# Optimization experiments

Measured on AMD Instinct MI355X. Metric: run time of the kernel, lower is better.

Reference implementation:

```python
import jax, jax.numpy as jnp
import numpy as np

B, S, D_IN, D_EMB, H = 2, 2048, 1024, 1024, 16
HD = D_EMB // H  # projection_dim = 64


def setup_inputs() -> dict:
    key = jax.random.key(0)
    ks = jax.random.split(key, 9)
    s_in = 1.0 / np.sqrt(D_IN)
    s_emb = 1.0 / np.sqrt(D_EMB)
    return {
        "inputs": jax.random.normal(ks[0], (B, S, D_IN), dtype=jnp.float32),
        "Wq": jax.random.uniform(ks[1], (D_IN, D_EMB), jnp.float32, -s_in, s_in),
        "bq": jax.random.uniform(ks[2], (D_EMB,), jnp.float32, -s_in, s_in),
        "Wk": jax.random.uniform(ks[3], (D_IN, D_EMB), jnp.float32, -s_in, s_in),
        "bk": jax.random.uniform(ks[4], (D_EMB,), jnp.float32, -s_in, s_in),
        "Wv": jax.random.uniform(ks[5], (D_IN, D_EMB), jnp.float32, -s_in, s_in),
        "bv": jax.random.uniform(ks[6], (D_EMB,), jnp.float32, -s_in, s_in),
        "Wo": jax.random.uniform(ks[7], (D_EMB, D_EMB), jnp.float32, -s_emb, s_emb),
        "bo": jax.random.uniform(ks[8], (D_EMB,), jnp.float32, -s_emb, s_emb),
    }


def reference(inputs, Wq, bq, Wk, bk, Wv, bv, Wo, bo):
    b, s, _ = inputs.shape
    # QKV projections -> [b, h, s, hd]
    def split_heads(x):
        return x.reshape(b, s, H, HD).transpose(0, 2, 1, 3)
    q = split_heads(inputs @ Wq + bq)
    k = split_heads(inputs @ Wk + bk)
    v = split_heads(inputs @ Wv + bv)
    scale = 1.0 / jnp.sqrt(jnp.float32(HD))
    logits = jnp.einsum('bhqd,bhkd->bhqk', q, k) * scale
    attn = jax.nn.softmax(logits, axis=-1)
    ctx = jnp.einsum('bhqk,bhkd->bhqd', attn, v)  # [b,h,s,hd]
    concat = ctx.transpose(0, 2, 1, 3).reshape(b, s, D_EMB)
    return concat @ Wo + bo
```

## Files before the change

### kernel.cpp

```cpp
#include <hip/hip_runtime.h>
#include <stdint.h>

#define S_ 2048
#define H_ 16

typedef short s16x8 __attribute__((ext_vector_type(8)));
typedef float f32x4 __attribute__((ext_vector_type(4)));
typedef float f32x16 __attribute__((ext_vector_type(16)));

__device__ __forceinline__ ushort f2bf(float f) {
    union { float f; uint32_t u; } v; v.f = f;
    uint32_t r = v.u + 0x7fffu + ((v.u >> 16) & 1u);
    return (ushort)(r >> 16);
}
__device__ __forceinline__ uint32_t cvtpk(float a, float b) {
    uint32_t r;
    asm("v_cvt_pk_bf16_f32 %0, %1, %2" : "=v"(r) : "v"(a), "v"(b));
    return r;
}
__device__ __forceinline__ void plswap(uint32_t& a, uint32_t& b) {
    auto r = __builtin_amdgcn_permlane32_swap((int)a, (int)b, false, false);
    a = (uint32_t)r[0];
    b = (uint32_t)r[1];
}
__device__ __forceinline__ float xmax32(float x) {
    uint32_t a = __float_as_uint(x), b = a;
    plswap(a, b);
    return fmaxf(__uint_as_float(a), __uint_as_float(b));
}
__device__ __forceinline__ float xadd32(float x) {
    uint32_t a = __float_as_uint(x), b = a;
    plswap(a, b);
    return __uint_as_float(a) + __uint_as_float(b);
}
__device__ __forceinline__ float exp2_fast(float x) {
    float r;
    asm("v_exp_f32 %0, %1" : "=v"(r) : "v"(x));
    return r;
}

__device__ __forceinline__ void gld16(ushort* lds, const ushort* g) {
    auto* gp = reinterpret_cast<uint32_t __attribute__((address_space(1)))*>(
        reinterpret_cast<uintptr_t>(g));
    auto* lp = reinterpret_cast<uint32_t __attribute__((address_space(3)))*>(
        reinterpret_cast<uintptr_t>(lds));
    __builtin_amdgcn_global_load_lds(gp, lp, 16, 0, 0);
}

__global__ void cast_bf16(const float* __restrict__ src, ushort* __restrict__ dst) {
    size_t i = ((size_t)blockIdx.x * 256 + threadIdx.x) * 8;
    float4 x = *(const float4*)(src + i);
    float4 y = *(const float4*)(src + i + 4);
    s16x8 r;
    r[0] = (short)f2bf(x.x); r[1] = (short)f2bf(x.y);
    r[2] = (short)f2bf(x.z); r[3] = (short)f2bf(x.w);
    r[4] = (short)f2bf(y.x); r[5] = (short)f2bf(y.y);
    r[6] = (short)f2bf(y.z); r[7] = (short)f2bf(y.w);
    *(s16x8*)(dst + i) = r;
}

__global__ void transpose_k4(const float* __restrict__ s0, const float* __restrict__ s1,
                             const float* __restrict__ s2, const float* __restrict__ s3,
                             ushort* __restrict__ d0, ushort* __restrict__ d1,
                             ushort* __restrict__ d2, ushort* __restrict__ d3) {
    const int z = blockIdx.z;
    const float* src = (z == 0) ? s0 : (z == 1) ? s1 : (z == 2) ? s2 : s3;
    ushort* dst      = (z == 0) ? d0 : (z == 1) ? d1 : (z == 2) ? d2 : d3;
    __shared__ ushort t[32][33];
    int bx = blockIdx.x * 32, by = blockIdx.y * 32;
    int x = threadIdx.x;
    for (int y = threadIdx.y; y < 32; y += 8)
        t[y][x] = f2bf(src[(size_t)(by + y) * 1024 + bx + x]);
    __syncthreads();
    for (int y = threadIdx.y; y < 32; y += 8)
        dst[(size_t)(bx + y) * 1024 + by + x] = t[x][y];
}

__global__ void gemm_bt(const ushort* __restrict__ A,
                        const ushort* __restrict__ Bt0, const ushort* __restrict__ Bt1,
                        const ushort* __restrict__ Bt2,
                        const float* __restrict__ bi0, const float* __restrict__ bi1,
                        const float* __restrict__ bi2,
                        void* __restrict__ o0, void* __restrict__ o1,
                        void* __restrict__ o2,
                        int mode0) {
    const int z = blockIdx.z;
    const ushort* Bt  = (z == 0) ? Bt0 : (z == 1) ? Bt1 : Bt2;
    const float* bia  = (z == 0) ? bi0 : (z == 1) ? bi1 : bi2;
    void* out         = (z == 0) ? o0  : (z == 1) ? o1  : o2;
    const int mode = mode0 + z;

    __shared__ __align__(16) ushort SMEM[2][4096];
    ushort* Asm = &SMEM[0][0];
    ushort* Bsm = &SMEM[1][0];

    const int t = threadIdx.x;
    const int lane = t & 63, w = t >> 6;
    const int wm = w >> 1, wn = w & 1;
    const int quad = lane >> 4, l16 = lane & 15;

    const int bid = blockIdx.y * 8 + blockIdx.x;
    const int swz = (bid & 7) * 32 + (bid >> 3);
    const int m0 = (swz >> 3) * 128, n0 = (swz & 7) * 128;
    const int K = 1024;

    const f32x4 FZ = {0.f, 0.f, 0.f, 0.f};
    f32x4 acc[4][4];
#pragma unroll
    for (int i = 0; i < 4; i++)
#pragma unroll
        for (int j = 0; j < 4; j++) acc[i][j] = FZ;

    const ushort* Ap = A  + (size_t)(m0 + (t >> 2)) * K + (t & 3) * 8;
    const ushort* Bp = Bt + (size_t)(n0 + (t >> 2)) * K + (t & 3) * 8;
    ushort* AsmW = Asm + w * 512;
    ushort* BsmW = Bsm + w * 512;

    for (int kt = 0; kt < K / 32; ++kt) {
        __syncthreads();
        gld16(AsmW,        Ap + kt * 32);
        gld16(AsmW + 2048, Ap + (size_t)64 * K + kt * 32);
        gld16(BsmW,        Bp + kt * 32);
        gld16(BsmW + 2048, Bp + (size_t)64 * K + kt * 32);
        __syncthreads();

        s16x8 a[4], b[4];
#pragma unroll
        for (int i = 0; i < 4; i++) {
            int row = wm * 64 + i * 16 + l16;
            a[i] = *(const s16x8*)((const char*)Asm + row * 64 + quad * 16);
        }
#pragma unroll
        for (int j = 0; j < 4; j++) {
            int row = wn * 64 + j * 16 + l16;
            b[j] = *(const s16x8*)((const char*)Bsm + row * 64 + quad * 16);
        }
#pragma unroll
        for (int i = 0; i < 4; i++)
#pragma unroll
            for (int j = 0; j < 4; j++)
                acc[i][j] = __builtin_amdgcn_mfma_f32_16x16x32_bf16(a[i], b[j], acc[i][j], 0, 0, 0);
    }

    if (mode == 3) {
        ushort* T = Asm;
        const int b_ = m0 >> 11;
        const int s_base = m0 & 2047;
        __syncthreads();
#pragma unroll
        for (int half = 0; half < 2; ++half) {
            if (wn == half) {
#pragma unroll
                for (int j = 0; j < 4; j++) {
                    int nl = j * 16 + l16;
                    float bv = bia[n0 + half * 64 + nl];
#pragma unroll
                    for (int i = 0; i < 4; i++) {
#pragma unroll
                        for (int r = 0; r < 4; r++) {
                            int ml = wm * 64 + i * 16 + quad * 4 + r;
                            T[nl * 128 + (ml ^ ((nl & 15) << 3))] = f2bf(acc[i][j][r] + bv);
                        }
                    }
                }
            }
            __syncthreads();
            {
                int row = t >> 2, cg = (t & 3) * 32;
                int ng = n0 + half * 64 + row;
                int h = ng >> 6, d = ng & 63;
                ushort* op = (ushort*)out + ((size_t)((b_ * 16 + h) * 64 + d)) * 2048 + s_base + cg;
#pragma unroll
                for (int c = 0; c < 4; c++) {
                    int col = (cg + c * 8) ^ ((row & 15) << 3);
                    *(s16x8*)(op + c * 8) = *(const s16x8*)(T + row * 128 + col);
                }
            }
            __syncthreads();
        }
        return;
    }

#pragma unroll
    for (int j = 0; j < 4; j++) {
        int n = n0 + wn * 64 + j * 16 + l16;
        float bv = bia[n];
#pragma unroll
        for (int i = 0; i < 4; i++) {
#pragma unroll
            for (int r = 0; r < 4; r++) {
                int m = m0 + wm * 64 + i * 16 + quad * 4 + r;
                float v = acc[i][j][r] + bv;
                if (mode == 0) {
                    ((float*)out)[(size_t)m * 1024 + n] = v;
                } else {
                    int b_ = m >> 11, s = m & 2047;
                    int h = n >> 6, d = n & 63;
                    if (mode == 1)
                        ((ushort*)out)[((size_t)(b_ * 16 + h) * 2048 + s) * 64 + d] = f2bf(v * 0.18033688011112042f);
                    else
                        ((ushort*)out)[((size_t)(b_ * 16 + h) * 2048 + s) * 64 + d] = f2bf(v);
                }
            }
        }
    }
}

#define MFMA32(a, b, c) __builtin_amdgcn_mfma_f32_32x32x16_bf16(a, b, c, 0, 0, 0)

__global__ __launch_bounds__(256, 2) void attn(const ushort* __restrict__ q_ws,
                                               const ushort* __restrict__ k_ws,
                                               const ushort* __restrict__ vt_ws,
                                               ushort* __restrict__ ctx) {
    __shared__ __align__(16) ushort Kb[2][4096];
    __shared__ __align__(16) ushort Vb[2][4096];
    __shared__ ushort obuf[4][32][72];

    const int t = threadIdx.x, lane = t & 63, w = t >> 6;
    const int l32 = lane & 31, hi = lane >> 5;

    const int bid = blockIdx.x;
    const int j_ = bid >> 3;
    const int bh = (bid & 7) + 8 * (j_ >> 4);
    const int q0 = (j_ & 15) * 128 + w * 32;

    const ushort* Qg = q_ws + (size_t)bh * S_ * 64;
    const ushort* Kg = k_ws + (size_t)bh * S_ * 64;
    const ushort* Vg = vt_ws + (size_t)bh * 64 * S_;

    s16x8 qf[4];
#pragma unroll
    for (int dc = 0; dc < 4; dc++)
        qf[dc] = *(const s16x8*)&Qg[(size_t)(q0 + l32) * 64 + dc * 16 + hi * 8];

    const int sr = t >> 3;
    const int sc = (t & 7) ^ (sr & 7);
    const ushort* kS = Kg + sr * 64 + sc * 8;
    const ushort* vS = Vg + (size_t)sr * 2048 + sc * 8;
    ushort* ldsK0 = &Kb[0][w * 512];
    ushort* ldsV0 = &Vb[0][w * 512];
    ushort* ldsK1 = &Kb[1][w * 512];
    ushort* ldsV1 = &Vb[1][w * 512];

    int fo[4];
#pragma unroll
    for (int c = 0; c < 4; c++)
        fo[c] = l32 * 64 + ((((c << 1) | hi) ^ (l32 & 7)) << 3);

    const f32x16 Z16 = {0.f,0.f,0.f,0.f,0.f,0.f,0.f,0.f,0.f,0.f,0.f,0.f,0.f,0.f,0.f,0.f};
    f32x16 o0 = Z16, o1 = Z16;
    float m_run = -1e30f, l_run = 0.f;

    gld16(ldsK0,        kS);
    gld16(ldsK0 + 2048, kS + 2048);
    gld16(ldsV0,        vS);
    gld16(ldsV0 + 2048, vS + (size_t)32 * 2048);
    __syncthreads();

    for (int kt = 0; kt < S_ / 64; ++kt) {
        const int cur = kt & 1;
        if (kt != S_ / 64 - 1) {
            const ushort* kn = kS + (kt + 1) * 4096;
            const ushort* vn = vS + (kt + 1) * 64;
            ushort* dK = cur ? ldsK0 : ldsK1;
            ushort* dV = cur ? ldsV0 : ldsV1;
            gld16(dK,        kn);
            gld16(dK + 2048, kn + 2048);
            gld16(dV,        vn);
            gld16(dV + 2048, vn + (size_t)32 * 2048);
        }
        const ushort* KB = &Kb[cur][0];
        const ushort* VB = &Vb[cur][0];

        f32x16 s0 = Z16, s1 = Z16;
        __builtin_amdgcn_s_setprio(1);
#pragma unroll
        for (int dc = 0; dc < 4; dc++) {
            s16x8 k0 = *(const s16x8*)(KB + fo[dc]);
            s16x8 k1 = *(const s16x8*)(KB + 2048 + fo[dc]);
            s0 = MFMA32(k0, qf[dc], s0);
            s1 = MFMA32(k1, qf[dc], s1);
        }
        __builtin_amdgcn_s_setprio(0);

        float m0 = fmaxf(s0[0], s1[0]), m1 = fmaxf(s0[1], s1[1]);
        float m2 = fmaxf(s0[2], s1[2]), m3 = fmaxf(s0[3], s1[3]);
#pragma unroll
        for (int r = 4; r < 16; r += 4) {
            m0 = fmaxf(m0, fmaxf(s0[r],     s1[r]));
            m1 = fmaxf(m1, fmaxf(s0[r + 1], s1[r + 1]));
            m2 = fmaxf(m2, fmaxf(s0[r + 2], s1[r + 2]));
            m3 = fmaxf(m3, fmaxf(s0[r + 3], s1[r + 3]));
        }
        float mx = fmaxf(fmaxf(m0, m1), fmaxf(m2, m3));
        mx = xmax32(mx);

        if (__any(mx > m_run + 8.f)) {
            float mnew = fmaxf(m_run, mx);
            float alpha = exp2_fast(m_run - mnew);
            m_run = mnew;
            l_run *= alpha;
#pragma unroll
            for (int r = 0; r < 16; r++) { o0[r] *= alpha; o1[r] *= alpha; }
        }

        float ra = 0.f, rb = 0.f;
#pragma unroll
        for (int r = 0; r < 16; r++) {
            s0[r] = exp2_fast(s0[r] - m_run); ra += s0[r];
            s1[r] = exp2_fast(s1[r] - m_run); rb += s1[r];
        }
        l_run += xadd32(ra + rb);

#pragma unroll
        for (int ks = 0; ks < 2; ks++) {
            const f32x16& p = ks ? s1 : s0;
            uint32_t u0 = cvtpk(p[0], p[1]),   u2 = cvtpk(p[4], p[5]);
            plswap(u0, u2);
            uint32_t u1 = cvtpk(p[2], p[3]),   u3 = cvtpk(p[6], p[7]);
            plswap(u1, u3);
            uint32_t w0 = cvtpk(p[8], p[9]),   w2 = cvtpk(p[12], p[13]);
            plswap(w0, w2);
            uint32_t w1 = cvtpk(p[10], p[11]), w3 = cvtpk(p[14], p[15]);
            plswap(w1, w3);
            union { uint32_t u[4]; s16x8 h; } F0, F1;
            F0.u[0] = u0; F0.u[1] = u1; F0.u[2] = u2; F0.u[3] = u3;
            F1.u[0] = w0; F1.u[1] = w1; F1.u[2] = w2; F1.u[3] = w3;

            const int kc0 = ks * 2, kc1 = ks * 2 + 1;
            s16x8 v00 = *(const s16x8*)(VB + fo[kc0]);
            s16x8 v01 = *(const s16x8*)(VB + 2048 + fo[kc0]);
            s16x8 v10 = *(const s16x8*)(VB + fo[kc1]);
            s16x8 v11 = *(const s16x8*)(VB + 2048 + fo[kc1]);
            __builtin_amdgcn_s_setprio(1);
            o0 = MFMA32(v00, F0.h, o0); o1 = MFMA32(v01, F0.h, o1);
            o0 = MFMA32(v10, F1.h, o0); o1 = MFMA32(v11, F1.h, o1);
            __builtin_amdgcn_s_setprio(0);
        }

        __syncthreads();
    }

    float inv = 1.0f / l_run;
#pragma unroll
    for (int r = 0; r < 16; r++) {
        int d0 = (r & 3) + 8 * (r >> 2) + 4 * hi;
        obuf[w][l32][d0]      = f2bf(o0[r] * inv);
        obuf[w][l32][32 + d0] = f2bf(o1[r] * inv);
    }
    asm volatile("s_waitcnt lgkmcnt(0)" ::: "memory");
    __builtin_amdgcn_sched_barrier(0);
    int b_ = bh >> 4, h = bh & 15;
    ushort* gp = ctx + ((size_t)(b_ * 2048 + q0 + l32)) * 1024 + h * 64 + hi * 32;
#pragma unroll
    for (int c = 0; c < 4; c++)
        *(s16x8*)(gp + c * 8) = *(const s16x8*)&obuf[w][l32][hi * 32 + c * 8];
}

extern "C" void kernel_launch(void* const* d_in, const int* in_sizes, int n_in,
                              void* d_out, int out_size, void* d_ws, size_t ws_size,
                              hipStream_t stream) {
    const float* X  = (const float*)d_in[0];
    const float* Wq = (const float*)d_in[1];
    const float* bq = (const float*)d_in[2];
    const float* Wk = (const float*)d_in[3];
    const float* bk = (const float*)d_in[4];
    const float* Wv = (const float*)d_in[5];
    const float* bv = (const float*)d_in[6];
    const float* Wo = (const float*)d_in[7];
    const float* bo = (const float*)d_in[8];
    float* out = (float*)d_out;

    char* ws = (char*)d_ws;
    ushort* wtq  = (ushort*)(ws);
    ushort* wtk  = (ushort*)(ws + ((size_t)2 << 20));
    ushort* wtv  = (ushort*)(ws + ((size_t)4 << 20));
    ushort* wto  = (ushort*)(ws + ((size_t)6 << 20));
    ushort* qws  = (ushort*)(ws + ((size_t)8 << 20));
    ushort* kws  = (ushort*)(ws + ((size_t)16 << 20));
    ushort* ctx  = (ushort*)(ws + ((size_t)24 << 20));
    ushort* vtws = (ushort*)d_out;
    ushort* xbf  = (ushort*)d_out + ((size_t)4 << 20);

    transpose_k4<<<dim3(32, 32, 4), dim3(32, 8), 0, stream>>>(Wq, Wk, Wv, Wo,
                                                              wtq, wtk, wtv, wto);
    cast_bf16<<<2048, 256, 0, stream>>>(X, xbf);

    gemm_bt<<<dim3(8, 32, 3), 256, 0, stream>>>(xbf, wtq, wtk, wtv, bq, bk, bv,
                                                qws, kws, vtws, 1);

    attn<<<dim3(512), 256, 0, stream>>>(qws, kws, vtws, ctx);

    gemm_bt<<<dim3(8, 32, 1), 256, 0, stream>>>(ctx, wto, wto, wto, bo, bo, bo,
                                                out, out, out, 0);
}
```

Measured before the change: 201.8 us.

## Widen GEMM K-tile to 64 with XOR-swizzled LDS layout

The projection GEMM now stages a 64-wide K slice per iteration instead of 32, halving the number of barrier-separated load/compute rounds. Global-to-LDS loads use an XOR swizzle on the 16-byte chunk index so fragment reads from LDS avoid bank conflicts with the wider 128-byte rows. It also adds launch bounds of 256 threads with a 4-block occupancy hint. LDS use doubles to 32 KB per block, which could limit occupancy, and there is still no double buffering.

```diff
diff --git a/kernel.cpp b/kernel.cpp
--- a/kernel.cpp
+++ b/kernel.cpp
@@ -76,23 +76,24 @@
         dst[(size_t)(bx + y) * 1024 + by + x] = t[x][y];
 }
 
-__global__ void gemm_bt(const ushort* __restrict__ A,
-                        const ushort* __restrict__ Bt0, const ushort* __restrict__ Bt1,
-                        const ushort* __restrict__ Bt2,
-                        const float* __restrict__ bi0, const float* __restrict__ bi1,
-                        const float* __restrict__ bi2,
-                        void* __restrict__ o0, void* __restrict__ o1,
-                        void* __restrict__ o2,
-                        int mode0) {
+#define MFMA16(a, b, c) __builtin_amdgcn_mfma_f32_16x16x32_bf16(a, b, c, 0, 0, 0)
+
+__global__ __launch_bounds__(256, 4) void gemm_bt(
+        const ushort* __restrict__ A,
+        const ushort* __restrict__ Bt0, const ushort* __restrict__ Bt1,
+        const ushort* __restrict__ Bt2,
+        const float* __restrict__ bi0, const float* __restrict__ bi1,
+        const float* __restrict__ bi2,
+        void* __restrict__ o0, void* __restrict__ o1, void* __restrict__ o2,
+        int mode0) {
     const int z = blockIdx.z;
     const ushort* Bt  = (z == 0) ? Bt0 : (z == 1) ? Bt1 : Bt2;
     const float* bia  = (z == 0) ? bi0 : (z == 1) ? bi1 : bi2;
     void* out         = (z == 0) ? o0  : (z == 1) ? o1  : o2;
     const int mode = mode0 + z;
 
-    __shared__ __align__(16) ushort SMEM[2][4096];
-    ushort* Asm = &SMEM[0][0];
-    ushort* Bsm = &SMEM[1][0];
+    __shared__ __align__(16) ushort Asm[128 * 64];
+    __shared__ __align__(16) ushort Bsm[128 * 64];
 
     const int t = threadIdx.x;
     const int lane = t & 63, w = t >> 6;
@@ -111,35 +112,41 @@
 #pragma unroll
         for (int j = 0; j < 4; j++) acc[i][j] = FZ;
 
-    const ushort* Ap = A  + (size_t)(m0 + (t >> 2)) * K + (t & 3) * 8;
-    const ushort* Bp = Bt + (size_t)(n0 + (t >> 2)) * K + (t & 3) * 8;
+    const int rr = t >> 3;
+    const int sc = (t & 7) ^ (rr & 7);
+    const ushort* Ap = A  + (size_t)(m0 + rr) * K + sc * 8;
+    const ushort* Bp = Bt + (size_t)(n0 + rr) * K + sc * 8;
     ushort* AsmW = Asm + w * 512;
     ushort* BsmW = Bsm + w * 512;
 
-    for (int kt = 0; kt < K / 32; ++kt) {
+    const int fx = l16 & 7;
+
+    for (int kt = 0; kt < 16; ++kt) {
         __syncthreads();
-        gld16(AsmW,        Ap + kt * 32);
-        gld16(AsmW + 2048, Ap + (size_t)64 * K + kt * 32);
-        gld16(BsmW,        Bp + kt * 32);
-        gld16(BsmW + 2048, Bp + (size_t)64 * K + kt * 32);
+        const int o = kt * 64;
+#pragma unroll
+        for (int g = 0; g < 4; g++) {
+            gld16(AsmW + g * 2048, Ap + (size_t)(g * 32) * K + o);
+            gld16(BsmW + g * 2048, Bp + (size_t)(g * 32) * K + o);
+        }
         __syncthreads();
 
-        s16x8 a[4], b[4];
-#pragma unroll
-        for (int i = 0; i < 4; i++) {
-            int row = wm * 64 + i * 16 + l16;
-            a[i] = *(const s16x8*)((const char*)Asm + row * 64 + quad * 16);
-        }
-#pragma unroll
-        for (int j = 0; j < 4; j++) {
-            int row = wn * 64 + j * 16 + l16;
-            b[j] = *(const s16x8*)((const char*)Bsm + row * 64 + quad * 16);
-        }
-#pragma unroll
-        for (int i = 0; i < 4; i++)
+#pragma unroll
+        for (int ks = 0; ks < 2; ks++) {
+            const int ck = (((ks << 2) | quad) ^ fx) * 8;
+            s16x8 a[4], b[4];
+#pragma unroll
+            for (int i = 0; i < 4; i++)
+                a[i] = *(const s16x8*)&Asm[(wm * 64 + i * 16 + l16) * 64 + ck];
 #pragma unroll
             for (int j = 0; j < 4; j++)
-                acc[i][j] = __builtin_amdgcn_mfma_f32_16x16x32_bf16(a[i], b[j], acc[i][j], 0, 0, 0);
+                b[j] = *(const s16x8*)&Bsm[(wn * 64 + j * 16 + l16) * 64 + ck];
+#pragma unroll
+            for (int i = 0; i < 4; i++)
+#pragma unroll
+                for (int j = 0; j < 4; j++)
+                    acc[i][j] = MFMA16(a[i], b[j], acc[i][j]);
+        }
     }
 
     if (mode == 3) {
```

New measurement: 193.7 us. 4.0% less time.
